# Kernel tuning notes

Hardware: AMD Instinct MI355X
Metric: run time of the kernel (lower is better)

The kernel has to match this reference:

```python
import jax, jax.numpy as jnp
import numpy as np

B, S, D, H = 2, 2048, 1024, 16
W = D // H  # head width = 64


def setup_inputs() -> dict:
    key = jax.random.key(0)
    ks = jax.random.split(key, 10)
    std = 1.0 / np.sqrt(D)
    return {
        "x": jax.random.normal(ks[0], (B, S, D), jnp.float32),
        "seg": jax.random.randint(ks[1], (B, S), 0, 2, jnp.int64),
        "Wq": jax.random.normal(ks[2], (D, D), jnp.float32) * std,
        "bq": jnp.zeros((D,), jnp.float32),
        "Wk": jax.random.normal(ks[3], (D, D), jnp.float32) * std,
        "bk": jnp.zeros((D,), jnp.float32),
        "Wv": jax.random.normal(ks[4], (D, D), jnp.float32) * std,
        "bv": jnp.zeros((D,), jnp.float32),
        "Wo": jax.random.normal(ks[5], (D, D), jnp.float32) * std,
        "bo": jnp.zeros((D,), jnp.float32),
    }


def reference(x, seg, Wq, bq, Wk, bk, Wv, bv, Wo, bo):
    # QKV projections: (B,S,D)
    q = x @ Wq + bq
    k = x @ Wk + bk
    v = x @ Wv + bv
    # split heads -> (B,H,S,W)
    def heads(t):
        return t.reshape(B, S, H, W).transpose(0, 2, 1, 3)
    q, k, v = heads(q), heads(k), heads(v)
    scale = 1.0 / np.sqrt(W).astype(np.float32)
    scores = jnp.einsum("bhqw,bhkw->bhqk", q, k) * scale  # (B,H,S,S)
    # causal mask: strictly-upper-triangular entries -> -inf
    causal = jnp.tril(jnp.ones((S, S), dtype=bool))
    scores = jnp.where(causal, scores, -jnp.inf)
    attn = jax.nn.softmax(scores, axis=-1)
    h = jnp.einsum("bhqk,bhkw->bhqw", attn, v)  # (B,H,S,W)
    h = h.transpose(0, 2, 1, 3).reshape(B, S, D)  # merge heads
    return h @ Wo + bo
```

## Files before the change

### kernel.cpp

```cpp
#include <hip/hip_runtime.h>

#define BB 2
#define SS 2048
#define DD 1024
#define HH 16
#define WW 64
#define MM (BB*SS)

typedef float f32x4 __attribute__((ext_vector_type(4)));
typedef short s16x8 __attribute__((ext_vector_type(8)));

__device__ __forceinline__ unsigned short f2bf(float f) {
  return __builtin_bit_cast(unsigned short, (__bf16)f);
}
__device__ __forceinline__ float bf2f(unsigned short u) {
  return (float)__builtin_bit_cast(__bf16, u);
}
__device__ __forceinline__ void dma16(const unsigned short* g, unsigned short* l) {
  __builtin_amdgcn_global_load_lds(
      (const __attribute__((address_space(1))) unsigned int*)g,
      (__attribute__((address_space(3))) unsigned int*)l, 16, 0, 0);
}

__global__ __launch_bounds__(256) void k_convert_x(const float* __restrict__ x,
                                                   unsigned short* __restrict__ xb) {
  int i = (blockIdx.x * 256 + threadIdx.x) * 4;
  float4 v = *(const float4*)(x + i);
  ushort4 o = make_ushort4(f2bf(v.x), f2bf(v.y), f2bf(v.z), f2bf(v.w));
  *(ushort4*)(xb + i) = o;
}

__global__ __launch_bounds__(256) void k_transpose_w(const float* __restrict__ W0,
                                                     const float* __restrict__ W1,
                                                     const float* __restrict__ W2,
                                                     const float* __restrict__ W3,
                                                     unsigned short* __restrict__ T0,
                                                     unsigned short* __restrict__ T1,
                                                     unsigned short* __restrict__ T2,
                                                     unsigned short* __restrict__ T3) {
  const float* Wm = blockIdx.z == 0 ? W0 : blockIdx.z == 1 ? W1 : blockIdx.z == 2 ? W2 : W3;
  unsigned short* Wt = blockIdx.z == 0 ? T0 : blockIdx.z == 1 ? T1 : blockIdx.z == 2 ? T2 : T3;
  __shared__ float tile[32][33];
  int bn = blockIdx.x * 32;
  int bk = blockIdx.y * 32;
  int tx = threadIdx.x;
  int ty = threadIdx.y;
#pragma unroll
  for (int r = 0; r < 4; ++r)
    tile[ty + r * 8][tx] = Wm[(bk + ty + r * 8) * DD + bn + tx];
  __syncthreads();
#pragma unroll
  for (int r = 0; r < 4; ++r)
    Wt[(bn + ty + r * 8) * DD + bk + tx] = f2bf(tile[tx][ty + r * 8]);
}

__global__ __launch_bounds__(256, 3) void k_gemm_qkv(const unsigned short* __restrict__ A,
                                                     const unsigned short* __restrict__ Wcat,
                                                     const float* __restrict__ bq,
                                                     const float* __restrict__ bk,
                                                     const float* __restrict__ bv,
                                                     unsigned short* __restrict__ Qo,
                                                     unsigned short* __restrict__ Ko,
                                                     unsigned short* __restrict__ Vo) {
  __shared__ __align__(16) unsigned short As[2][128 * 32];
  __shared__ __align__(16) unsigned short Bs[2][128 * 32];
  const int widx = blockIdx.x >> 3;
  const int n0 = (blockIdx.x & 7) * 128;
  const int m0 = blockIdx.y * 128;
  const unsigned short* Bt = Wcat + (size_t)widx * DD * DD;
  const float* bias = widx == 0 ? bq : widx == 1 ? bk : bv;
  unsigned short* outp = widx == 0 ? Qo : widx == 1 ? Ko : Vo;
  const float oscale = widx == 0 ? 0.125f * 1.4426950408889634f : 1.0f;
  const int t = threadIdx.x;
  const int wv = t >> 6, lane = t & 63;
  const int quad = lane >> 4, l16 = lane & 15;
  const int wm = (wv >> 1) * 64, wn = (wv & 1) * 64;
  const unsigned short* srcA[2];
  const unsigned short* srcB[2];
  int dstoff[2];
#pragma unroll
  for (int d = 0; d < 2; ++d) {
    int s = d * 256 + wv * 64 + lane;
    int r = s >> 2, pb = s & 3;
    int lc = ((pb ^ (r & 3)) << 3);
    srcA[d] = A + (size_t)(m0 + r) * DD + lc;
    srcB[d] = Bt + (size_t)(n0 + r) * DD + lc;
    dstoff[d] = (d * 256 + wv * 64) * 8;
  }
  f32x4 acc[4][4] = {};

#pragma unroll
  for (int d = 0; d < 2; ++d) {
    dma16(srcA[d], &As[0][dstoff[d]]);
    dma16(srcB[d], &Bs[0][dstoff[d]]);
  }

  for (int it = 0; it < DD / 32; ++it) {
    asm volatile("s_waitcnt vmcnt(0)" ::: "memory");
    __syncthreads();
    if (it + 1 < DD / 32) {
      const int nb = (it + 1) & 1;
      const int k1 = (it + 1) * 32;
#pragma unroll
      for (int d = 0; d < 2; ++d) {
        dma16(srcA[d] + k1, &As[nb][dstoff[d]]);
        dma16(srcB[d] + k1, &Bs[nb][dstoff[d]]);
      }
    }
    const unsigned short* Asb = As[it & 1];
    const unsigned short* Bsb = Bs[it & 1];
    s16x8 af[4], bfr[4];
#pragma unroll
    for (int mi = 0; mi < 4; ++mi) {
      int ra = wm + mi * 16 + l16;
      af[mi] = *(const s16x8*)(Asb + ra * 32 + ((quad ^ (ra & 3)) << 3));
    }
#pragma unroll
    for (int ni = 0; ni < 4; ++ni) {
      int rb = wn + ni * 16 + l16;
      bfr[ni] = *(const s16x8*)(Bsb + rb * 32 + ((quad ^ (rb & 3)) << 3));
    }
#pragma unroll
    for (int mi = 0; mi < 4; ++mi)
#pragma unroll
      for (int ni = 0; ni < 4; ++ni)
        acc[mi][ni] = __builtin_amdgcn_mfma_f32_16x16x32_bf16(af[mi], bfr[ni], acc[mi][ni], 0, 0, 0);
  }

#pragma unroll
  for (int mi = 0; mi < 4; ++mi) {
#pragma unroll
    for (int ni = 0; ni < 4; ++ni) {
      int col = n0 + wn + ni * 16 + l16;
      float bb = bias[col];
      int h = col >> 6, w = col & 63;
#pragma unroll
      for (int r = 0; r < 4; ++r) {
        int row = m0 + wm + mi * 16 + quad * 4 + r;
        float v = (acc[mi][ni][r] + bb) * oscale;
        int b = row >> 11, s = row & (SS - 1);
        long off;
        if (widx == 2) off = (long)(b * HH + h) * (SS * WW) + (long)w * SS + s;
        else           off = (long)(b * HH + h) * (SS * WW) + (long)s * WW + w;
        outp[off] = f2bf(v);
      }
    }
  }
}

__global__ __launch_bounds__(256, 4) void k_gemm_out(const unsigned short* __restrict__ A,
                                                     const unsigned short* __restrict__ Bt,
                                                     const float* __restrict__ bias,
                                                     float* __restrict__ out_f) {
  __shared__ __align__(16) unsigned short As[2][64 * 32];
  __shared__ __align__(16) unsigned short Bs[2][64 * 32];
  const int m0 = blockIdx.y * 64, n0 = blockIdx.x * 64;
  const int t = threadIdx.x;
  const int wv = t >> 6, lane = t & 63;
  const int quad = lane >> 4, l16 = lane & 15;
  const int wm = (wv >> 1) * 32, wn = (wv & 1) * 32;
  const int s_ = wv * 64 + lane;
  const int r_ = s_ >> 2, pb_ = s_ & 3;
  const int lc_ = ((pb_ ^ (r_ & 3)) << 3);
  const unsigned short* srcA = A + (size_t)(m0 + r_) * DD + lc_;
  const unsigned short* srcB = Bt + (size_t)(n0 + r_) * DD + lc_;
  const int dstoff = wv * 512;
  f32x4 acc[2][2] = {};

  dma16(srcA, &As[0][dstoff]);
  dma16(srcB, &Bs[0][dstoff]);

  for (int it = 0; it < DD / 32; ++it) {
    asm volatile("s_waitcnt vmcnt(0)" ::: "memory");
    __syncthreads();
    if (it + 1 < DD / 32) {
      const int nb = (it + 1) & 1;
      const int k1 = (it + 1) * 32;
      dma16(srcA + k1, &As[nb][dstoff]);
      dma16(srcB + k1, &Bs[nb][dstoff]);
    }
    const unsigned short* Asb = As[it & 1];
    const unsigned short* Bsb = Bs[it & 1];
    s16x8 af[2], bfr[2];
#pragma unroll
    for (int i = 0; i < 2; ++i) {
      int ra = wm + i * 16 + l16;
      int rb = wn + i * 16 + l16;
      af[i]  = *(const s16x8*)(Asb + ra * 32 + ((quad ^ (ra & 3)) << 3));
      bfr[i] = *(const s16x8*)(Bsb + rb * 32 + ((quad ^ (rb & 3)) << 3));
    }
#pragma unroll
    for (int mi = 0; mi < 2; ++mi)
#pragma unroll
      for (int ni = 0; ni < 2; ++ni)
        acc[mi][ni] = __builtin_amdgcn_mfma_f32_16x16x32_bf16(af[mi], bfr[ni], acc[mi][ni], 0, 0, 0);
  }

#pragma unroll
  for (int mi = 0; mi < 2; ++mi)
#pragma unroll
    for (int ni = 0; ni < 2; ++ni) {
      int col = n0 + wn + ni * 16 + l16;
      float bb = bias[col];
#pragma unroll
      for (int r = 0; r < 4; ++r) {
        int row = m0 + wm + mi * 16 + quad * 4 + r;
        out_f[row * DD + col] = acc[mi][ni][r] + bb;
      }
    }
}

__global__ __launch_bounds__(256, 1) void k_attn_mfma(const unsigned short* __restrict__ Q,
                                                      const unsigned short* __restrict__ K,
                                                      const unsigned short* __restrict__ Vt,
                                                      unsigned short* __restrict__ hm) {
  constexpr int LDP = 136;
  __shared__ __align__(16) unsigned short Kbuf[2][128 * 64];
  __shared__ __align__(16) unsigned short Vbuf[2][64 * 128];
  __shared__ __align__(16) unsigned short Pl4[4][32 * LDP];
  const int pairp = blockIdx.x;
  const int bh = blockIdx.y;
  const int t = threadIdx.x;
  const int wv = t >> 6, lane = t & 63;
  const int quad = lane >> 4, l16 = lane & 15;
  unsigned short* Pl = Pl4[wv];
  const unsigned short* Qp = Q + (size_t)bh * SS * WW;
  const unsigned short* Kp = K + (size_t)bh * SS * WW;
  const unsigned short* Vp = Vt + (size_t)bh * WW * SS;
  const int b = bh >> 4, h = bh & 15;

  const int rrK = lane >> 3;
  const int kswz = (((lane & 7) ^ rrK) << 3);

  for (int sp = 0; sp < 2; ++sp) {
    const int strip = sp == 0 ? pairp : 15 - pairp;
    const int qs = strip * 128;
    const int qb = qs + wv * 32;

    s16x8 qf[2][2];
#pragma unroll
    for (int nt = 0; nt < 2; ++nt)
#pragma unroll
      for (int c = 0; c < 2; ++c)
        qf[nt][c] = *(const s16x8*)(Qp + (qb + nt * 16 + l16) * WW + c * 32 + quad * 8);

    f32x4 O[2][4] = {};
    float m[2], l[2];
    m[0] = m[1] = -__builtin_inff();
    l[0] = l[1] = 0.f;

    const int nkt = qs / 128 + 1;

#pragma unroll
    for (int d = 0; d < 4; ++d) {
      const int D = wv * 4 + d;
      dma16(Kp + (size_t)(D * 8 + rrK) * WW + kswz, &Kbuf[0][D * 512]);
      const int vrow = D * 4 + quad;
      dma16(Vp + (size_t)vrow * SS + (((lane & 15) ^ (vrow & 7)) << 3), &Vbuf[0][D * 512]);
    }

    for (int kt = 0; kt < nkt; ++kt) {
      const int kb = kt * 128;
      asm volatile("s_waitcnt vmcnt(0)" ::: "memory");
      __syncthreads();
      if (kt + 1 < nkt) {
        const int nb = (kt + 1) & 1;
        const int kbn = kb + 128;
#pragma unroll
        for (int d = 0; d < 4; ++d) {
          const int D = wv * 4 + d;
          dma16(Kp + (size_t)(kbn + D * 8 + rrK) * WW + kswz, &Kbuf[nb][D * 512]);
          const int vrow = D * 4 + quad;
          dma16(Vp + (size_t)vrow * SS + kbn + (((lane & 15) ^ (vrow & 7)) << 3),
                &Vbuf[nb][D * 512]);
        }
      }
      const unsigned short* Kb_ = Kbuf[kt & 1];
      const unsigned short* Vb_ = Vbuf[kt & 1];

      s16x8 kf[8][2];
#pragma unroll
      for (int mt = 0; mt < 8; ++mt)
#pragma unroll
        for (int c = 0; c < 2; ++c)
          kf[mt][c] = *(const s16x8*)(Kb_ + (mt * 16 + l16) * 64 + (((c * 4 + quad) ^ (l16 & 7)) << 3));

      f32x4 sc[8][2] = {};
#pragma unroll
      for (int mt = 0; mt < 8; ++mt)
#pragma unroll
        for (int nt = 0; nt < 2; ++nt)
#pragma unroll
          for (int c = 0; c < 2; ++c)
            sc[mt][nt] = __builtin_amdgcn_mfma_f32_16x16x32_bf16(kf[mt][c], qf[nt][c], sc[mt][nt], 0, 0, 0);

      if (kt == nkt - 1) {
#pragma unroll
        for (int mt = 0; mt < 8; ++mt)
#pragma unroll
          for (int nt = 0; nt < 2; ++nt)
#pragma unroll
            for (int r = 0; r < 4; ++r)
              if (kb + mt * 16 + quad * 4 + r > qb + nt * 16 + l16)
                sc[mt][nt][r] = -__builtin_inff();
      }

      float alpha[2];
#pragma unroll
      for (int nt = 0; nt < 2; ++nt) {
        float mx = sc[0][nt][0];
#pragma unroll
        for (int mt = 0; mt < 8; ++mt)
#pragma unroll
          for (int r = 0; r < 4; ++r) mx = fmaxf(mx, sc[mt][nt][r]);
        mx = fmaxf(mx, __shfl_xor(mx, 16));
        mx = fmaxf(mx, __shfl_xor(mx, 32));
        float mn = fmaxf(m[nt], mx);
        alpha[nt] = __builtin_amdgcn_exp2f(m[nt] - mn);
        float s = 0.f;
#pragma unroll
        for (int mt = 0; mt < 8; ++mt)
#pragma unroll
          for (int r = 0; r < 4; ++r) {
            float p = __builtin_amdgcn_exp2f(sc[mt][nt][r] - mn);
            sc[mt][nt][r] = p;
            s += p;
          }
        s += __shfl_xor(s, 16);
        s += __shfl_xor(s, 32);
        l[nt] = l[nt] * alpha[nt] + s;
        m[nt] = mn;
      }

#pragma unroll
      for (int mi = 0; mi < 2; ++mi)
#pragma unroll
        for (int r = 0; r < 4; ++r) {
          float aT = __shfl(alpha[mi], quad * 4 + r);
#pragma unroll
          for (int ni = 0; ni < 4; ++ni) O[mi][ni][r] *= aT;
        }

      asm volatile("s_waitcnt lgkmcnt(0)" ::: "memory");
#pragma unroll
      for (int mt = 0; mt < 8; ++mt)
#pragma unroll
        for (int nt = 0; nt < 2; ++nt) {
          ushort4 pw = make_ushort4(f2bf(sc[mt][nt][0]), f2bf(sc[mt][nt][1]),
                                    f2bf(sc[mt][nt][2]), f2bf(sc[mt][nt][3]));
          *(ushort4*)(Pl + (nt * 16 + l16) * LDP + mt * 16 + quad * 4) = pw;
        }
      asm volatile("s_waitcnt lgkmcnt(0)" ::: "memory");

      s16x8 vf[4][4];
#pragma unroll
      for (int ni = 0; ni < 4; ++ni)
#pragma unroll
        for (int c = 0; c < 4; ++c)
          vf[ni][c] = *(const s16x8*)(Vb_ + (ni * 16 + l16) * 128 + (((c * 4 + quad) ^ (l16 & 7)) << 3));

      s16x8 pf[2][4];
#pragma unroll
      for (int mi = 0; mi < 2; ++mi)
#pragma unroll
        for (int c = 0; c < 4; ++c)
          pf[mi][c] = *(const s16x8*)(Pl + (mi * 16 + l16) * LDP + c * 32 + quad * 8);

#pragma unroll
      for (int mi = 0; mi < 2; ++mi)
#pragma unroll
        for (int ni = 0; ni < 4; ++ni)
#pragma unroll
          for (int c = 0; c < 4; ++c)
            O[mi][ni] = __builtin_amdgcn_mfma_f32_16x16x32_bf16(pf[mi][c], vf[ni][c], O[mi][ni], 0, 0, 0);
    }

#pragma unroll
    for (int mi = 0; mi < 2; ++mi)
#pragma unroll
      for (int r = 0; r < 4; ++r) {
        float linv = 1.f / __shfl(l[mi], quad * 4 + r);
        int q = qb + mi * 16 + quad * 4 + r;
#pragma unroll
        for (int ni = 0; ni < 4; ++ni)
          hm[(size_t)(b * SS + q) * DD + h * WW + ni * 16 + l16] = f2bf(O[mi][ni][r] * linv);
      }
    __syncthreads();
  }
}

extern "C" void kernel_launch(void* const* d_in, const int* in_sizes, int n_in,
                              void* d_out, int out_size, void* d_ws, size_t ws_size,
                              hipStream_t stream) {
  const float* x  = (const float*)d_in[0];
  const float* Wq = (const float*)d_in[2];
  const float* bq = (const float*)d_in[3];
  const float* Wk = (const float*)d_in[4];
  const float* bk = (const float*)d_in[5];
  const float* Wv = (const float*)d_in[6];
  const float* bv = (const float*)d_in[7];
  const float* Wo = (const float*)d_in[8];
  const float* bo = (const float*)d_in[9];
  float* out = (float*)d_out;

  char* ws = (char*)d_ws;
  unsigned short* xb   = (unsigned short*)(ws);
  unsigned short* Wcat = (unsigned short*)(ws + (size_t)( 8 << 20));
  unsigned short* Wtq  = Wcat;
  unsigned short* Wtk  = Wcat + (size_t)DD * DD;
  unsigned short* Wtv  = Wcat + (size_t)2 * DD * DD;
  unsigned short* Wto  = (unsigned short*)(ws + (size_t)(14 << 20));
  unsigned short* Qb   = (unsigned short*)(ws + (size_t)(16 << 20));
  unsigned short* Kb   = (unsigned short*)(ws + (size_t)(24 << 20));
  unsigned short* Vtb  = (unsigned short*)(ws + (size_t)(32 << 20));
  unsigned short* hm   = (unsigned short*)(ws + (size_t)(40 << 20));

  k_convert_x<<<dim3(MM * DD / 1024), 256, 0, stream>>>(x, xb);

  dim3 tg(32, 32, 4), tb(32, 8);
  k_transpose_w<<<tg, tb, 0, stream>>>(Wq, Wk, Wv, Wo, Wtq, Wtk, Wtv, Wto);

  dim3 gq(24, MM / 128);
  k_gemm_qkv<<<gq, 256, 0, stream>>>(xb, Wcat, bq, bk, bv, Qb, Kb, Vtb);

  dim3 ag(SS / 256, BB * HH);
  k_attn_mfma<<<ag, 256, 0, stream>>>(Qb, Kb, Vtb, hm);

  dim3 go(DD / 64, MM / 64);
  k_gemm_out<<<go, 256, 0, stream>>>(hm, Wto, bo, out);
}
```

Baseline: 210.7 us.

## Keep attention P in registers and halve query rows per block

The attention kernel now processes 16 query rows per wave (64 per block) and doubles the grid, so each K/V tile is loaded for half as many queries, but there are twice as many blocks to fill the CUs. The probability matrix is packed straight from the score accumulators into MFMA operands, with V fragments gathered by two 4-element LDS reads that match that layout. This removes the per-wave P staging buffer in LDS and its waitcnts. Launch bounds now allow two blocks per CU. K/V tile traffic roughly doubles in exchange for lower LDS use and register pressure.

```diff
diff --git a/kernel.cpp b/kernel.cpp
--- a/kernel.cpp
+++ b/kernel.cpp
@@ -9,6 +9,7 @@
 
 typedef float f32x4 __attribute__((ext_vector_type(4)));
 typedef short s16x8 __attribute__((ext_vector_type(8)));
+typedef short s16x4 __attribute__((ext_vector_type(4)));
 
 __device__ __forceinline__ unsigned short f2bf(float f) {
   return __builtin_bit_cast(unsigned short, (__bf16)f);
@@ -210,20 +211,18 @@
     }
 }
 
-__global__ __launch_bounds__(256, 1) void k_attn_mfma(const unsigned short* __restrict__ Q,
+__global__ __launch_bounds__(256, 2) void k_attn_mfma(const unsigned short* __restrict__ Q,
                                                       const unsigned short* __restrict__ K,
                                                       const unsigned short* __restrict__ Vt,
                                                       unsigned short* __restrict__ hm) {
-  constexpr int LDP = 136;
   __shared__ __align__(16) unsigned short Kbuf[2][128 * 64];
   __shared__ __align__(16) unsigned short Vbuf[2][64 * 128];
-  __shared__ __align__(16) unsigned short Pl4[4][32 * LDP];
-  const int pairp = blockIdx.x;
+  const int pairp = blockIdx.x >> 1;
+  const int qh = blockIdx.x & 1;
   const int bh = blockIdx.y;
   const int t = threadIdx.x;
   const int wv = t >> 6, lane = t & 63;
   const int quad = lane >> 4, l16 = lane & 15;
-  unsigned short* Pl = Pl4[wv];
   const unsigned short* Qp = Q + (size_t)bh * SS * WW;
   const unsigned short* Kp = K + (size_t)bh * SS * WW;
   const unsigned short* Vp = Vt + (size_t)bh * WW * SS;
@@ -235,21 +234,18 @@
   for (int sp = 0; sp < 2; ++sp) {
     const int strip = sp == 0 ? pairp : 15 - pairp;
     const int qs = strip * 128;
-    const int qb = qs + wv * 32;
-
-    s16x8 qf[2][2];
-#pragma unroll
-    for (int nt = 0; nt < 2; ++nt)
-#pragma unroll
-      for (int c = 0; c < 2; ++c)
-        qf[nt][c] = *(const s16x8*)(Qp + (qb + nt * 16 + l16) * WW + c * 32 + quad * 8);
-
-    f32x4 O[2][4] = {};
-    float m[2], l[2];
-    m[0] = m[1] = -__builtin_inff();
-    l[0] = l[1] = 0.f;
-
-    const int nkt = qs / 128 + 1;
+    const int qb = qs + qh * 64 + wv * 16;
+
+    s16x8 qf[2];
+#pragma unroll
+    for (int c = 0; c < 2; ++c)
+      qf[c] = *(const s16x8*)(Qp + (qb + l16) * WW + c * 32 + quad * 8);
+
+    f32x4 O[4] = {};
+    float m = -__builtin_inff();
+    float l = 0.f;
+
+    const int nkt = strip + 1;
 
 #pragma unroll
     for (int d = 0; d < 4; ++d) {
@@ -285,106 +281,86 @@
         for (int c = 0; c < 2; ++c)
           kf[mt][c] = *(const s16x8*)(Kb_ + (mt * 16 + l16) * 64 + (((c * 4 + quad) ^ (l16 & 7)) << 3));
 
-      f32x4 sc[8][2] = {};
+      f32x4 sc[8] = {};
 #pragma unroll
       for (int mt = 0; mt < 8; ++mt)
 #pragma unroll
-        for (int nt = 0; nt < 2; ++nt)
-#pragma unroll
-          for (int c = 0; c < 2; ++c)
-            sc[mt][nt] = __builtin_amdgcn_mfma_f32_16x16x32_bf16(kf[mt][c], qf[nt][c], sc[mt][nt], 0, 0, 0);
+        for (int c = 0; c < 2; ++c)
+          sc[mt] = __builtin_amdgcn_mfma_f32_16x16x32_bf16(kf[mt][c], qf[c], sc[mt], 0, 0, 0);
 
       if (kt == nkt - 1) {
 #pragma unroll
         for (int mt = 0; mt < 8; ++mt)
 #pragma unroll
-          for (int nt = 0; nt < 2; ++nt)
-#pragma unroll
-            for (int r = 0; r < 4; ++r)
-              if (kb + mt * 16 + quad * 4 + r > qb + nt * 16 + l16)
-                sc[mt][nt][r] = -__builtin_inff();
-      }
-
-      float alpha[2];
-#pragma unroll
-      for (int nt = 0; nt < 2; ++nt) {
-        float mx = sc[0][nt][0];
-#pragma unroll
-        for (int mt = 0; mt < 8; ++mt)
-#pragma unroll
-          for (int r = 0; r < 4; ++r) mx = fmaxf(mx, sc[mt][nt][r]);
-        mx = fmaxf(mx, __shfl_xor(mx, 16));
-        mx = fmaxf(mx, __shfl_xor(mx, 32));
-        float mn = fmaxf(m[nt], mx);
-        alpha[nt] = __builtin_amdgcn_exp2f(m[nt] - mn);
-        float s = 0.f;
-#pragma unroll
-        for (int mt = 0; mt < 8; ++mt)
-#pragma unroll
-          for (int r = 0; r < 4; ++r) {
-            float p = __builtin_amdgcn_exp2f(sc[mt][nt][r] - mn);
-            sc[mt][nt][r] = p;
-            s += p;
-          }
-        s += __shfl_xor(s, 16);
-        s += __shfl_xor(s, 32);
-        l[nt] = l[nt] * alpha[nt] + s;
-        m[nt] = mn;
-      }
-
-#pragma unroll
-      for (int mi = 0; mi < 2; ++mi)
+          for (int r = 0; r < 4; ++r)
+            if (kb + mt * 16 + quad * 4 + r > qb + l16)
+              sc[mt][r] = -__builtin_inff();
+      }
+
+      float mx = sc[0][0];
+#pragma unroll
+      for (int mt = 0; mt < 8; ++mt)
+#pragma unroll
+        for (int r = 0; r < 4; ++r) mx = fmaxf(mx, sc[mt][r]);
+      mx = fmaxf(mx, __shfl_xor(mx, 16));
+      mx = fmaxf(mx, __shfl_xor(mx, 32));
+      const float mn = fmaxf(m, mx);
+      const float alpha = __builtin_amdgcn_exp2f(m - mn);
+      float s = 0.f;
+#pragma unroll
+      for (int mt = 0; mt < 8; ++mt)
 #pragma unroll
         for (int r = 0; r < 4; ++r) {
-          float aT = __shfl(alpha[mi], quad * 4 + r);
-#pragma unroll
-          for (int ni = 0; ni < 4; ++ni) O[mi][ni][r] *= aT;
+          float p = __builtin_amdgcn_exp2f(sc[mt][r] - mn);
+          sc[mt][r] = p;
+          s += p;
         }
-
-      asm volatile("s_waitcnt lgkmcnt(0)" ::: "memory");
-#pragma unroll
-      for (int mt = 0; mt < 8; ++mt)
-#pragma unroll
-        for (int nt = 0; nt < 2; ++nt) {
-          ushort4 pw = make_ushort4(f2bf(sc[mt][nt][0]), f2bf(sc[mt][nt][1]),
-                                    f2bf(sc[mt][nt][2]), f2bf(sc[mt][nt][3]));
-          *(ushort4*)(Pl + (nt * 16 + l16) * LDP + mt * 16 + quad * 4) = pw;
+      s += __shfl_xor(s, 16);
+      s += __shfl_xor(s, 32);
+      l = l * alpha + s;
+      m = mn;
+
+#pragma unroll
+      for (int r = 0; r < 4; ++r) {
+        const float aT = __shfl(alpha, quad * 4 + r);
+#pragma unroll
+        for (int ni = 0; ni < 4; ++ni) O[ni][r] *= aT;
+      }
+
+      s16x8 pf[4];
+#pragma unroll
+      for (int c = 0; c < 4; ++c) {
+#pragma unroll
+        for (int e = 0; e < 4; ++e) {
+          pf[c][e]     = (short)f2bf(sc[2 * c][e]);
+          pf[c][4 + e] = (short)f2bf(sc[2 * c + 1][e]);
         }
-      asm volatile("s_waitcnt lgkmcnt(0)" ::: "memory");
-
-      s16x8 vf[4][4];
+      }
+
+      const int xr = l16 & 7;
+#pragma unroll
+      for (int ni = 0; ni < 4; ++ni) {
+        const unsigned short* vrp = Vb_ + (ni * 16 + l16) * 128 + ((quad & 1) << 2);
+#pragma unroll
+        for (int c = 0; c < 4; ++c) {
+          const int blo = (4 * c + (quad >> 1)) ^ xr;
+          const int bhi = (4 * c + 2 + (quad >> 1)) ^ xr;
+          s16x4 vlo = *(const s16x4*)(vrp + (blo << 3));
+          s16x4 vhi = *(const s16x4*)(vrp + (bhi << 3));
+          s16x8 vfc = __builtin_shufflevector(vlo, vhi, 0, 1, 2, 3, 4, 5, 6, 7);
+          O[ni] = __builtin_amdgcn_mfma_f32_16x16x32_bf16(pf[c], vfc, O[ni], 0, 0, 0);
+        }
+      }
+    }
+
+#pragma unroll
+    for (int r = 0; r < 4; ++r) {
+      const float linv = 1.f / __shfl(l, quad * 4 + r);
+      const int q = qb + quad * 4 + r;
 #pragma unroll
       for (int ni = 0; ni < 4; ++ni)
-#pragma unroll
-        for (int c = 0; c < 4; ++c)
-          vf[ni][c] = *(const s16x8*)(Vb_ + (ni * 16 + l16) * 128 + (((c * 4 + quad) ^ (l16 & 7)) << 3));
-
-      s16x8 pf[2][4];
-#pragma unroll
-      for (int mi = 0; mi < 2; ++mi)
-#pragma unroll
-        for (int c = 0; c < 4; ++c)
-          pf[mi][c] = *(const s16x8*)(Pl + (mi * 16 + l16) * LDP + c * 32 + quad * 8);
-
-#pragma unroll
-      for (int mi = 0; mi < 2; ++mi)
-#pragma unroll
-        for (int ni = 0; ni < 4; ++ni)
-#pragma unroll
-          for (int c = 0; c < 4; ++c)
-            O[mi][ni] = __builtin_amdgcn_mfma_f32_16x16x32_bf16(pf[mi][c], vf[ni][c], O[mi][ni], 0, 0, 0);
-    }
-
-#pragma unroll
-    for (int mi = 0; mi < 2; ++mi)
-#pragma unroll
-      for (int r = 0; r < 4; ++r) {
-        float linv = 1.f / __shfl(l[mi], quad * 4 + r);
-        int q = qb + mi * 16 + quad * 4 + r;
-#pragma unroll
-        for (int ni = 0; ni < 4; ++ni)
-          hm[(size_t)(b * SS + q) * DD + h * WW + ni * 16 + l16] = f2bf(O[mi][ni][r] * linv);
-      }
+        hm[(size_t)(b * SS + q) * DD + h * WW + ni * 16 + l16] = f2bf(O[ni][r] * linv);
+    }
     __syncthreads();
   }
 }
@@ -423,7 +399,7 @@
   dim3 gq(24, MM / 128);
   k_gemm_qkv<<<gq, 256, 0, stream>>>(xb, Wcat, bq, bk, bv, Qb, Kb, Vtb);
 
-  dim3 ag(SS / 256, BB * HH);
+  dim3 ag(16, BB * HH);
   k_attn_mfma<<<ag, 256, 0, stream>>>(Qb, Kb, Vtb, hm);
 
   dim3 go(DD / 64, MM / 64);
```

Result: faster. 203.6 us (-3.4%).
